# Performance work log

Measured on AMD Instinct MI355X. Metric: run time of the kernel, lower is better.

## Reference

```python
import jax, jax.numpy as jnp
import numpy as np

NUM_HEADS = 8
EPS = 1e-6


def hamilton(a, b):
    # Quaternion (Hamilton) product on the last axis (size 4), broadcasting leading dims.
    aw, ax, ay, az = a[..., 0], a[..., 1], a[..., 2], a[..., 3]
    bw, bx, by, bz = b[..., 0], b[..., 1], b[..., 2], b[..., 3]
    return jnp.stack([
        aw * bw - ax * bx - ay * by - az * bz,
        aw * bx + ax * bw + ay * bz - az * by,
        aw * by - ax * bz + ay * bw + az * bx,
        aw * bz + ax * by - ay * bx + az * bw,
    ], axis=-1)


def setup_inputs() -> dict:
    key = jax.random.key(0)
    ks = jax.random.split(key, 7)
    B, L, E = 2, 384, 512
    s = 1.0 / np.sqrt(E)
    return {
        'x': jax.random.normal(ks[0], (B, L, E), dtype=jnp.float32),
        'Wq': jax.random.normal(ks[1], (E, E), dtype=jnp.float32) * s,
        'Wk': jax.random.normal(ks[2], (E, E), dtype=jnp.float32) * s,
        'Wv': jax.random.normal(ks[3], (E, E), dtype=jnp.float32) * s,
        'Wo': jax.random.normal(ks[4], (E, E), dtype=jnp.float32) * s,
        'dde_w': jax.random.normal(ks[5], (4, 4), dtype=jnp.float32) * 0.5,
        'dde_b': jnp.zeros((4,), dtype=jnp.float32),
    }


def reference(x, Wq, Wk, Wv, Wo, dde_w, dde_b):
    B, L, E = x.shape
    H = NUM_HEADS
    hd = E // H            # head_dim
    c = hd // 4            # quaternion atoms per head

    def proj_quat(W):
        # x @ W^T  -> split heads -> quaternion atoms: (B*H, L, c, 4)
        y = jnp.einsum('ble,fe->blf', x, W)
        y = y.reshape(B, L, H, hd).transpose(0, 2, 1, 3)  # (B,H,L,hd)
        return y.reshape(B * H, L, c, 4)

    q = proj_quat(Wq)
    k = proj_quat(Wk)
    v = proj_quat(Wv)

    # Broadcasted Hamilton product: (BH, L, L, c, 4)
    interference = hamilton(q[:, :, None, :, :], k[:, None, :, :, :])
    norm = jnp.linalg.norm(interference, axis=-1, keepdims=True) + EPS
    spinor = interference / norm

    # Discrete decision gate: mean over atoms -> (BH, L, L, 4) -> sigmoid(linear)
    gate_in = spinor.mean(axis=-2)
    gate = jax.nn.sigmoid(jnp.einsum('blmq,pq->blmp', gate_in, dde_w) + dde_b)
    spinor = spinor * gate[:, :, :, None, :]

    # Value aggregation: Hamilton product with v, summed over key positions j
    ctx = hamilton(spinor, v[:, None, :, :, :]).sum(axis=2)  # (BH, L, c, 4)

    ctx = ctx.reshape(B, H, L, hd).transpose(0, 2, 1, 3).reshape(B, L, E)
    return jnp.einsum('ble,fe->blf', ctx, Wo)
```

## Files before the change

kernel.cpp:

```cpp
#include <hip/hip_runtime.h>
#include <math.h>

#define L_SEQ 384
#define E_DIM 512
#define NHEAD 8
#define NBH   16
#define HD    64
#define LOG2E 1.44269504f

typedef __attribute__((ext_vector_type(8))) __bf16 bf16x8;
typedef __attribute__((ext_vector_type(8))) _Float16 f16x8;
typedef __attribute__((ext_vector_type(4))) float f32x4;

union u4h8 { uint4 u; f16x8 h; };

__device__ __forceinline__ float uniform_f(float v) {
  return __uint_as_float(__builtin_amdgcn_readfirstlane(__float_as_uint(v)));
}

__device__ __forceinline__ unsigned f2bf(float f) {
  unsigned u = __float_as_uint(f);
  return (u + 0x7FFFu + ((u >> 16) & 1u)) >> 16;
}

__device__ __forceinline__ unsigned ror16(unsigned x) { return (x >> 16) | (x << 16); }

__device__ __forceinline__ float dpp_xor1(float x) {
  return __int_as_float(__builtin_amdgcn_mov_dpp(__float_as_int(x), 0xB1, 0xF, 0xF, 0));
}
__device__ __forceinline__ float dpp_xor2(float x) {
  return __int_as_float(__builtin_amdgcn_mov_dpp(__float_as_int(x), 0x4E, 0xF, 0xF, 0));
}
template <int IMM>
__device__ __forceinline__ float swz_xor(float x) {
  return __int_as_float(__builtin_amdgcn_ds_swizzle(__float_as_int(x), IMM));
}

__device__ __forceinline__ size_t pidx(int row, int k, int Kd) {
  return ((((size_t)(row >> 4) * (Kd >> 5) + (k >> 5)) * 4 + ((k >> 3) & 3)) * 16
          + (row & 15)) * 8 + (k & 7);
}

__global__ __launch_bounds__(256) void to_bf16_all(
    const float* __restrict__ x, const float* __restrict__ Wq,
    const float* __restrict__ Wk, const float* __restrict__ Wv,
    const float* __restrict__ Wo, unsigned short* __restrict__ dst1,
    unsigned short* __restrict__ dst2, float* __restrict__ outz)
{
  int e0 = (blockIdx.x * 256 + threadIdx.x) * 4;
  if (e0 >= 1835008) return;
  if (e0 >= 1441792) {
    *(float4*)(outz + (e0 - 1441792)) = make_float4(0.f, 0.f, 0.f, 0.f);
    return;
  }
  const float* src; unsigned short* d; int s;
  if (e0 < 393216)       { src = x;  s = e0;           d = dst1; }
  else if (e0 < 655360)  { src = Wq; s = e0 - 393216;  d = dst1 + 393216; }
  else if (e0 < 917504)  { src = Wk; s = e0 - 655360;  d = dst1 + 655360; }
  else if (e0 < 1179648) { src = Wv; s = e0 - 917504;  d = dst1 + 917504; }
  else                   { src = Wo; s = e0 - 1179648; d = dst2; }
  float4 v = *(const float4*)(src + s);
  unsigned lo = f2bf(v.x) | (f2bf(v.y) << 16);
  unsigned hi = f2bf(v.z) | (f2bf(v.w) << 16);
  int row = s >> 9, k = s & 511;
  *(uint2*)(d + pidx(row, k, 512)) = make_uint2(lo, hi);
}

template <int NTN, int MODE>
__global__ __launch_bounds__(256) void gemm_mfma(
    const __bf16* __restrict__ A, const __bf16* __restrict__ B0,
    const __bf16* __restrict__ B1, const __bf16* __restrict__ B2,
    float* __restrict__ C0, float* __restrict__ C1, float* __restrict__ C2,
    int M, int N, int K)
{
  const int z = blockIdx.z;
  const __bf16* Bm = (MODE == 2) ? B0 : (z == 0) ? B0 : (z == 1) ? B1 : B2;
  float* Cp = (MODE == 2) ? C0 : (z == 0) ? C0 : (z == 1) ? C1 : C2;

  const int tid = threadIdx.x;
  const int wave = tid >> 6, lane = tid & 63;
  const int m0 = blockIdx.y * 64 + wave * 16;
  const int n0 = blockIdx.x * (16 * NTN);
  const int mr = lane & 15, quad = lane >> 4;
  const int KT = K >> 5;
  const int kb0 = (MODE == 2) ? z * 4 : 0;
  const int KL = (MODE == 2) ? 4 : KT;

  f32x4 acc[NTN];
  #pragma unroll
  for (int nt = 0; nt < NTN; ++nt) acc[nt] = (f32x4){0.f, 0.f, 0.f, 0.f};

  const __bf16* ap = A + ((size_t)(m0 >> 4) * KT + kb0) * 512 + lane * 8;
  const __bf16* bp = Bm + ((size_t)(n0 >> 4) * KT + kb0) * 512 + lane * 8;

  #pragma unroll 4
  for (int ks = 0; ks < KL; ++ks) {
    bf16x8 a = *(const bf16x8*)(ap + (size_t)ks * 512);
    #pragma unroll
    for (int nt = 0; nt < NTN; ++nt) {
      bf16x8 b = *(const bf16x8*)(bp + ((size_t)nt * KT + ks) * 512);
      acc[nt] = __builtin_amdgcn_mfma_f32_16x16x32_bf16(a, b, acc[nt], 0, 0, 0);
    }
  }

  if (MODE == 2) {
    #pragma unroll
    for (int nt = 0; nt < NTN; ++nt) {
      int n = n0 + nt * 16 + mr;
      #pragma unroll
      for (int r = 0; r < 4; ++r) {
        int m = m0 + quad * 4 + r;
        __hip_atomic_fetch_add(&Cp[(size_t)m * N + n], acc[nt][r],
                               __ATOMIC_RELAXED, __HIP_MEMORY_SCOPE_AGENT);
      }
    }
  } else {
    _Float16* Hp = (_Float16*)Cp;
    #pragma unroll
    for (int nt = 0; nt < NTN; ++nt) {
      int n = n0 + nt * 16 + mr;
      #pragma unroll
      for (int r = 0; r < 4; ++r) {
        float val = acc[nt][r];
        float s = val * val;
        s += dpp_xor1(s);
        s += dpp_xor2(s);
        float sc = (z == 2) ? 1.f : __builtin_amdgcn_rsqf(fmaxf(s, 1e-30f));
        int m = m0 + quad * 4 + r;
        int b = m / L_SEQ, l = m - b * L_SEQ;
        int row = (b * NHEAD + (n >> 6)) * L_SEQ + l;
        Hp[pidx(row, n & 63, 64)] = (_Float16)(val * sc);
      }
    }
  }
}

__global__ __launch_bounds__(256) void z_build(
    const _Float16* __restrict__ khh, const _Float16* __restrict__ vhh,
    _Float16* __restrict__ Z0)
{
  const int tid = threadIdx.x;
  const int l = blockIdx.x * 64 + (tid & 63);
  const int a = blockIdx.y * 4 + (tid >> 6);
  const int bh = blockIdx.z;

  size_t off = pidx(bh * L_SEQ + l, a * 4, 64);
  union { uint2 u; _Float16 h[4]; } kk, vv;
  kk.u = *(const uint2*)(khh + off);
  vv.u = *(const uint2*)(vhh + off);

  float kb[4] = {(float)kk.h[0], (float)kk.h[1], (float)kk.h[2], (float)kk.h[3]};
  float ve[4] = {(float)vv.h[0], (float)vv.h[1], (float)vv.h[2], (float)vv.h[3]};
  _Float16* zp = Z0 + (size_t)bh * (256 * 384);
  #pragma unroll
  for (int b = 0; b < 4; ++b)
    #pragma unroll
    for (int e = 0; e < 4; ++e)
      zp[pidx(a * 16 + b * 4 + e, l, 384)] = (_Float16)(kb[b] * ve[e]);
}

__global__ __launch_bounds__(256) void score_gate(
    const _Float16* __restrict__ qhh, const _Float16* __restrict__ khh,
    const float* __restrict__ dde_w, const float* __restrict__ dde_b,
    _Float16* __restrict__ G)
{
  const int tid = threadIdx.x, wave = tid >> 6, lane = tid & 63;
  const int mr = lane & 15, quad = lane >> 4;
  const int bh = blockIdx.z;
  const int i0 = blockIdx.y * 64 + wave * 16;
  const int j0 = blockIdx.x * 32;

  float wn[16], bn[4];
  #pragma unroll
  for (int t = 0; t < 16; ++t) wn[t] = uniform_f(dde_w[t]) * (-LOG2E * 0.0625f);
  #pragma unroll
  for (int c = 0; c < 4; ++c) bn[c] = uniform_f(dde_b[c]) * (-LOG2E);

  f32x4 acc[4][2];
  #pragma unroll
  for (int c = 0; c < 4; ++c)
    #pragma unroll
    for (int nt = 0; nt < 2; ++nt) acc[c][nt] = (f32x4){0.f, 0.f, 0.f, 0.f};

  const _Float16* ap = qhh + (size_t)((bh * L_SEQ + i0) >> 4) * 2 * 512 + lane * 8;
  const _Float16* bp = khh + (size_t)((bh * L_SEQ + j0) >> 4) * 2 * 512 + lane * 8;

  #pragma unroll
  for (int ks = 0; ks < 2; ++ks) {
    uint4 qa = *(const uint4*)(ap + ks * 512);
    unsigned s0 = ror16(qa.x), s1 = ror16(qa.y), s2 = ror16(qa.z), s3 = ror16(qa.w);
    u4h8 fr[4];
    fr[0].u = make_uint4(qa.x ^ 0x80000000u, qa.y ^ 0x80008000u,
                         qa.z ^ 0x80000000u, qa.w ^ 0x80008000u);
    fr[1].u = make_uint4(s0, s1 ^ 0x00008000u, s2, s3 ^ 0x00008000u);
    fr[2].u = make_uint4(qa.y, qa.x ^ 0x80000000u, qa.w, qa.z ^ 0x80000000u);
    fr[3].u = make_uint4(s1 ^ 0x80000000u, s0, s3 ^ 0x80000000u, s2);
    #pragma unroll
    for (int nt = 0; nt < 2; ++nt) {
      u4h8 bb; bb.h = *(const f16x8*)(bp + ((size_t)nt * 2 + ks) * 512);
      #pragma unroll
      for (int c = 0; c < 4; ++c)
        acc[c][nt] = __builtin_amdgcn_mfma_f32_16x16x32_f16(fr[c].h, bb.h, acc[c][nt], 0, 0, 0);
    }
  }

  #pragma unroll
  for (int nt = 0; nt < 2; ++nt) {
    const int j = j0 + nt * 16 + mr;
    #pragma unroll
    for (int r = 0; r < 4; ++r) {
      const int i = i0 + quad * 4 + r;
      float S0 = acc[0][nt][r], S1 = acc[1][nt][r];
      float S2 = acc[2][nt][r], S3 = acc[3][nt][r];
      #pragma unroll
      for (int c = 0; c < 4; ++c) {
        float n = bn[c] + wn[c*4+0]*S0 + wn[c*4+1]*S1 + wn[c*4+2]*S2 + wn[c*4+3]*S3;
        float g = __builtin_amdgcn_rcpf(1.f + __builtin_amdgcn_exp2f(n));
        G[(size_t)(c * NBH + bh) * (384 * 384) + pidx(i, j, 384)] = (_Float16)g;
      }
    }
  }
}

__global__ __launch_bounds__(256) void pv_combine(
    const _Float16* __restrict__ G, const _Float16* __restrict__ Z0,
    const _Float16* __restrict__ qhh, unsigned short* __restrict__ CTXB)
{
  __shared__ float qs[16][17];
  __shared__ float vxs[4][4][16][4];
  const int tid = threadIdx.x, c = tid >> 6, lane = tid & 63;
  const int mr = lane & 15, quad = lane >> 4;
  const int bh = blockIdx.z;
  const int i0 = blockIdx.x * 16;
  const int cg = blockIdx.y;

  {
    int il = tid >> 4, t = tid & 15;
    qs[il][t] = (float)qhh[pidx(bh * L_SEQ + i0 + il, cg * 16 + t, 64)];
  }
  __syncthreads();

  const int bq = mr >> 2, e = mr & 3;
  const unsigned msk =
      ((((0x284Eu >> (c * 4 + bq)) ^ (0xC6A0u >> (c * 4 + e))) & 1u) << 31);

  f32x4 acc[4];
  #pragma unroll
  for (int nt = 0; nt < 4; ++nt) acc[nt] = (f32x4){0.f, 0.f, 0.f, 0.f};

  const _Float16* apg = G + (size_t)(c * NBH + bh) * (384 * 384)
                          + (size_t)(i0 >> 4) * 12 * 512 + lane * 8;
  const _Float16* bpz = Z0 + (size_t)bh * (256 * 384)
                           + (size_t)(cg * 4) * 12 * 512 + lane * 8;

  #pragma unroll 4
  for (int ks = 0; ks < 12; ++ks) {
    u4h8 aa; aa.h = *(const f16x8*)(apg + (size_t)ks * 512);
    #pragma unroll
    for (int nt = 0; nt < 4; ++nt) {
      u4h8 bb; bb.h = *(const f16x8*)(bpz + ((size_t)nt * 12 + ks) * 512);
      acc[nt] = __builtin_amdgcn_mfma_f32_16x16x32_f16(aa.h, bb.h, acc[nt], 0, 0, 0);
    }
  }

  #pragma unroll
  for (int nt = 0; nt < 4; ++nt) {
    #pragma unroll
    for (int r = 0; r < 4; ++r) {
      int il = quad * 4 + r;
      float sq = __uint_as_float(__float_as_uint(qs[il][nt * 4 + (bq ^ c)]) ^ msk);
      float v = sq * acc[nt][r];
      v += swz_xor<0x101F>(v);
      v += swz_xor<0x201F>(v);
      if (bq == 0) vxs[c][e][il][nt] = v;
    }
  }
  __syncthreads();

  {
    int il = tid >> 4, cc = tid & 15, nt = cc >> 2, d = cc & 3;
    float s = vxs[0][d][il][nt] + vxs[1][1 ^ d][il][nt] +
              vxs[2][2 ^ d][il][nt] + vxs[3][3 ^ d][il][nt];
    int bb_ = bh >> 3, hh = bh & 7;
    CTXB[pidx(bb_ * L_SEQ + i0 + il, hh * HD + cg * 16 + nt * 4 + d, 512)] =
        (unsigned short)f2bf(s);
  }
}

extern "C" void kernel_launch(void* const* d_in, const int* in_sizes, int n_in,
                              void* d_out, int out_size, void* d_ws, size_t ws_size,
                              hipStream_t stream)
{
  const float* x     = (const float*)d_in[0];
  const float* Wq    = (const float*)d_in[1];
  const float* Wk    = (const float*)d_in[2];
  const float* Wv    = (const float*)d_in[3];
  const float* Wo    = (const float*)d_in[4];
  const float* dde_w = (const float*)d_in[5];
  const float* dde_b = (const float*)d_in[6];
  float* out = (float*)d_out;

  char* ws = (char*)d_ws;
  unsigned short* Wob  = (unsigned short*)(ws + 0);
  _Float16* qhh = (_Float16*)(ws + 524288);
  _Float16* khh = (_Float16*)(ws + 1310720);
  unsigned short* CTXB = (unsigned short*)(ws + 1310720);
  _Float16* Z0h = (_Float16*)(ws + 2097152);
  _Float16* Gh  = (_Float16*)(ws + 5242880);
  _Float16* vhh = (_Float16*)(ws + 5242880);
  unsigned short* xb  = (unsigned short*)(ws + 6029312);
  unsigned short* Wqb = (unsigned short*)(ws + 6815744);
  unsigned short* Wkb = (unsigned short*)(ws + 7340032);
  unsigned short* Wvb = (unsigned short*)(ws + 7864320);

  to_bf16_all<<<1792, 256, 0, stream>>>(x, Wq, Wk, Wv, Wo, xb, Wob, out);

  gemm_mfma<2, 1><<<dim3(16, 12, 3), 256, 0, stream>>>(
      (const __bf16*)xb, (const __bf16*)Wqb, (const __bf16*)Wkb, (const __bf16*)Wvb,
      (float*)qhh, (float*)khh, (float*)vhh, 2 * L_SEQ, E_DIM, E_DIM);

  z_build<<<dim3(6, 4, 16), 256, 0, stream>>>(khh, vhh, Z0h);

  score_gate<<<dim3(12, 6, 16), 256, 0, stream>>>(qhh, khh, dde_w, dde_b, Gh);

  pv_combine<<<dim3(24, 4, 16), 256, 0, stream>>>(Gh, Z0h, qhh, CTXB);

  gemm_mfma<2, 2><<<dim3(16, 12, 4), 256, 0, stream>>>(
      (const __bf16*)CTXB, (const __bf16*)Wob, nullptr, nullptr,
      out, nullptr, nullptr, 2 * L_SEQ, E_DIM, E_DIM);
}
```

Before: 112.2 us.

## Fuse score-gate and PV combine into one kernel with gates in LDS

Merges the score_gate and pv_combine kernels so each block computes the sigmoid gate tile for its 16 query rows chunk by chunk into shared memory and feeds it straight into the PV MFMAs. This removes the global gate tensor of shape 4x16x384x384 in fp16 and its write/read round trip, plus one launch. In exchange the score MFMAs are recomputed once per column group (4x redundant) and two barriers are added per chunk. The QKV projection GEMM tile config is also changed to launch twice as many blocks.

```diff
diff --git a/kernel.cpp b/kernel.cpp
--- a/kernel.cpp
+++ b/kernel.cpp
@@ -159,16 +159,24 @@
       zp[pidx(a * 16 + b * 4 + e, l, 384)] = (_Float16)(kb[b] * ve[e]);
 }
 
-__global__ __launch_bounds__(256) void score_gate(
+__global__ __launch_bounds__(256) void gate_pv(
     const _Float16* __restrict__ qhh, const _Float16* __restrict__ khh,
-    const float* __restrict__ dde_w, const float* __restrict__ dde_b,
-    _Float16* __restrict__ G)
-{
-  const int tid = threadIdx.x, wave = tid >> 6, lane = tid & 63;
+    const _Float16* __restrict__ Z0, const float* __restrict__ dde_w,
+    const float* __restrict__ dde_b, unsigned short* __restrict__ CTXB)
+{
+  __shared__ _Float16 gbuf[4096];
+  __shared__ float vxs[4][4][16][4];
+  __shared__ float qs[16][17];
+
+  const int tid = threadIdx.x, w = tid >> 6, lane = tid & 63;
   const int mr = lane & 15, quad = lane >> 4;
-  const int bh = blockIdx.z;
-  const int i0 = blockIdx.y * 64 + wave * 16;
-  const int j0 = blockIdx.x * 32;
+  const int bh = blockIdx.z, cg = blockIdx.y, ib = blockIdx.x;
+  const int i0 = ib * 16;
+
+  {
+    int il = tid >> 4, t = tid & 15;
+    qs[il][t] = (float)qhh[pidx(bh * L_SEQ + i0 + il, cg * 16 + t, 64)];
+  }
 
   float wn[16], bn[4];
   #pragma unroll
@@ -176,91 +184,73 @@
   #pragma unroll
   for (int c = 0; c < 4; ++c) bn[c] = uniform_f(dde_b[c]) * (-LOG2E);
 
-  f32x4 acc[4][2];
-  #pragma unroll
-  for (int c = 0; c < 4; ++c)
-    #pragma unroll
-    for (int nt = 0; nt < 2; ++nt) acc[c][nt] = (f32x4){0.f, 0.f, 0.f, 0.f};
-
-  const _Float16* ap = qhh + (size_t)((bh * L_SEQ + i0) >> 4) * 2 * 512 + lane * 8;
-  const _Float16* bp = khh + (size_t)((bh * L_SEQ + j0) >> 4) * 2 * 512 + lane * 8;
-
-  #pragma unroll
-  for (int ks = 0; ks < 2; ++ks) {
-    uint4 qa = *(const uint4*)(ap + ks * 512);
-    unsigned s0 = ror16(qa.x), s1 = ror16(qa.y), s2 = ror16(qa.z), s3 = ror16(qa.w);
-    u4h8 fr[4];
-    fr[0].u = make_uint4(qa.x ^ 0x80000000u, qa.y ^ 0x80008000u,
-                         qa.z ^ 0x80000000u, qa.w ^ 0x80008000u);
-    fr[1].u = make_uint4(s0, s1 ^ 0x00008000u, s2, s3 ^ 0x00008000u);
-    fr[2].u = make_uint4(qa.y, qa.x ^ 0x80000000u, qa.w, qa.z ^ 0x80000000u);
-    fr[3].u = make_uint4(s1 ^ 0x80000000u, s0, s3 ^ 0x80000000u, s2);
-    #pragma unroll
-    for (int nt = 0; nt < 2; ++nt) {
-      u4h8 bb; bb.h = *(const f16x8*)(bp + ((size_t)nt * 2 + ks) * 512);
-      #pragma unroll
-      for (int c = 0; c < 4; ++c)
-        acc[c][nt] = __builtin_amdgcn_mfma_f32_16x16x32_f16(fr[c].h, bb.h, acc[c][nt], 0, 0, 0);
-    }
-  }
-
-  #pragma unroll
-  for (int nt = 0; nt < 2; ++nt) {
-    const int j = j0 + nt * 16 + mr;
+  u4h8 fr[4][2];
+  {
+    const _Float16* ap = qhh + ((size_t)(bh * 24 + ib)) * 2 * 512 + lane * 8;
+    #pragma unroll
+    for (int ks = 0; ks < 2; ++ks) {
+      uint4 qa = *(const uint4*)(ap + ks * 512);
+      unsigned s0 = ror16(qa.x), s1 = ror16(qa.y), s2 = ror16(qa.z), s3 = ror16(qa.w);
+      fr[0][ks].u = make_uint4(qa.x ^ 0x80000000u, qa.y ^ 0x80008000u,
+                               qa.z ^ 0x80000000u, qa.w ^ 0x80008000u);
+      fr[1][ks].u = make_uint4(s0, s1 ^ 0x00008000u, s2, s3 ^ 0x00008000u);
+      fr[2][ks].u = make_uint4(qa.y, qa.x ^ 0x80000000u, qa.w, qa.z ^ 0x80000000u);
+      fr[3][ks].u = make_uint4(s1 ^ 0x80000000u, s0, s3 ^ 0x80000000u, s2);
+    }
+  }
+
+  const int bq = mr >> 2, e = mr & 3;
+  const unsigned msk =
+      ((((0x284Eu >> (w * 4 + bq)) ^ (0xC6A0u >> (w * 4 + e))) & 1u) << 31);
+
+  f32x4 acc[4];
+  #pragma unroll
+  for (int nt = 0; nt < 4; ++nt) acc[nt] = (f32x4){0.f, 0.f, 0.f, 0.f};
+
+  const int jl = w * 16 + mr;
+  const int gw = (jl >> 3) * 128 + (jl & 7) + quad * 32;
+
+  for (int ch = 0; ch < 6; ++ch) {
+    u4h8 zb[2][4];
+    #pragma unroll
+    for (int ks2 = 0; ks2 < 2; ++ks2)
+      #pragma unroll
+      for (int nt = 0; nt < 4; ++nt)
+        zb[ks2][nt].h = *(const f16x8*)(Z0 + (size_t)bh * (256 * 384)
+                         + (((size_t)(cg * 4 + nt) * 12 + ch * 2 + ks2) * 512) + lane * 8);
+
+    const _Float16* bp = khh + ((size_t)(bh * 24 + ch * 4 + w)) * 2 * 512 + lane * 8;
+    u4h8 kb[2];
+    kb[0].h = *(const f16x8*)(bp);
+    kb[1].h = *(const f16x8*)(bp + 512);
+    f32x4 accS[4];
+    #pragma unroll
+    for (int c = 0; c < 4; ++c) {
+      accS[c] = (f32x4){0.f, 0.f, 0.f, 0.f};
+      accS[c] = __builtin_amdgcn_mfma_f32_16x16x32_f16(fr[c][0].h, kb[0].h, accS[c], 0, 0, 0);
+      accS[c] = __builtin_amdgcn_mfma_f32_16x16x32_f16(fr[c][1].h, kb[1].h, accS[c], 0, 0, 0);
+    }
+
     #pragma unroll
     for (int r = 0; r < 4; ++r) {
-      const int i = i0 + quad * 4 + r;
-      float S0 = acc[0][nt][r], S1 = acc[1][nt][r];
-      float S2 = acc[2][nt][r], S3 = acc[3][nt][r];
+      float S0 = accS[0][r], S1 = accS[1][r], S2 = accS[2][r], S3 = accS[3][r];
       #pragma unroll
       for (int c = 0; c < 4; ++c) {
         float n = bn[c] + wn[c*4+0]*S0 + wn[c*4+1]*S1 + wn[c*4+2]*S2 + wn[c*4+3]*S3;
         float g = __builtin_amdgcn_rcpf(1.f + __builtin_amdgcn_exp2f(n));
-        G[(size_t)(c * NBH + bh) * (384 * 384) + pidx(i, j, 384)] = (_Float16)g;
+        gbuf[c * 1024 + gw + r * 8] = (_Float16)g;
       }
     }
-  }
-}
-
-__global__ __launch_bounds__(256) void pv_combine(
-    const _Float16* __restrict__ G, const _Float16* __restrict__ Z0,
-    const _Float16* __restrict__ qhh, unsigned short* __restrict__ CTXB)
-{
-  __shared__ float qs[16][17];
-  __shared__ float vxs[4][4][16][4];
-  const int tid = threadIdx.x, c = tid >> 6, lane = tid & 63;
-  const int mr = lane & 15, quad = lane >> 4;
-  const int bh = blockIdx.z;
-  const int i0 = blockIdx.x * 16;
-  const int cg = blockIdx.y;
-
-  {
-    int il = tid >> 4, t = tid & 15;
-    qs[il][t] = (float)qhh[pidx(bh * L_SEQ + i0 + il, cg * 16 + t, 64)];
-  }
-  __syncthreads();
-
-  const int bq = mr >> 2, e = mr & 3;
-  const unsigned msk =
-      ((((0x284Eu >> (c * 4 + bq)) ^ (0xC6A0u >> (c * 4 + e))) & 1u) << 31);
-
-  f32x4 acc[4];
-  #pragma unroll
-  for (int nt = 0; nt < 4; ++nt) acc[nt] = (f32x4){0.f, 0.f, 0.f, 0.f};
-
-  const _Float16* apg = G + (size_t)(c * NBH + bh) * (384 * 384)
-                          + (size_t)(i0 >> 4) * 12 * 512 + lane * 8;
-  const _Float16* bpz = Z0 + (size_t)bh * (256 * 384)
-                           + (size_t)(cg * 4) * 12 * 512 + lane * 8;
-
-  #pragma unroll 4
-  for (int ks = 0; ks < 12; ++ks) {
-    u4h8 aa; aa.h = *(const f16x8*)(apg + (size_t)ks * 512);
-    #pragma unroll
-    for (int nt = 0; nt < 4; ++nt) {
-      u4h8 bb; bb.h = *(const f16x8*)(bpz + ((size_t)nt * 12 + ks) * 512);
-      acc[nt] = __builtin_amdgcn_mfma_f32_16x16x32_f16(aa.h, bb.h, acc[nt], 0, 0, 0);
-    }
+    __syncthreads();
+
+    #pragma unroll
+    for (int ks2 = 0; ks2 < 2; ++ks2) {
+      f16x8 aa = *(const f16x8*)&gbuf[(w * 2 + ks2) * 512 + lane * 8];
+      #pragma unroll
+      for (int nt = 0; nt < 4; ++nt)
+        acc[nt] = __builtin_amdgcn_mfma_f32_16x16x32_f16(aa, zb[ks2][nt].h, acc[nt], 0, 0, 0);
+    }
+    __syncthreads();
   }
 
   #pragma unroll
@@ -268,11 +258,11 @@
     #pragma unroll
     for (int r = 0; r < 4; ++r) {
       int il = quad * 4 + r;
-      float sq = __uint_as_float(__float_as_uint(qs[il][nt * 4 + (bq ^ c)]) ^ msk);
+      float sq = __uint_as_float(__float_as_uint(qs[il][nt * 4 + (bq ^ w)]) ^ msk);
       float v = sq * acc[nt][r];
       v += swz_xor<0x101F>(v);
       v += swz_xor<0x201F>(v);
-      if (bq == 0) vxs[c][e][il][nt] = v;
+      if (bq == 0) vxs[w][e][il][nt] = v;
     }
   }
   __syncthreads();
@@ -304,10 +294,9 @@
   unsigned short* Wob  = (unsigned short*)(ws + 0);
   _Float16* qhh = (_Float16*)(ws + 524288);
   _Float16* khh = (_Float16*)(ws + 1310720);
-  unsigned short* CTXB = (unsigned short*)(ws + 1310720);
   _Float16* Z0h = (_Float16*)(ws + 2097152);
-  _Float16* Gh  = (_Float16*)(ws + 5242880);
   _Float16* vhh = (_Float16*)(ws + 5242880);
+  unsigned short* CTXB = (unsigned short*)(ws + 5242880);
   unsigned short* xb  = (unsigned short*)(ws + 6029312);
   unsigned short* Wqb = (unsigned short*)(ws + 6815744);
   unsigned short* Wkb = (unsigned short*)(ws + 7340032);
@@ -315,15 +304,13 @@
 
   to_bf16_all<<<1792, 256, 0, stream>>>(x, Wq, Wk, Wv, Wo, xb, Wob, out);
 
-  gemm_mfma<2, 1><<<dim3(16, 12, 3), 256, 0, stream>>>(
+  gemm_mfma<1, 1><<<dim3(32, 12, 3), 256, 0, stream>>>(
       (const __bf16*)xb, (const __bf16*)Wqb, (const __bf16*)Wkb, (const __bf16*)Wvb,
       (float*)qhh, (float*)khh, (float*)vhh, 2 * L_SEQ, E_DIM, E_DIM);
 
   z_build<<<dim3(6, 4, 16), 256, 0, stream>>>(khh, vhh, Z0h);
 
-  score_gate<<<dim3(12, 6, 16), 256, 0, stream>>>(qhh, khh, dde_w, dde_b, Gh);
-
-  pv_combine<<<dim3(24, 4, 16), 256, 0, stream>>>(Gh, Z0h, qhh, CTXB);
+  gate_pv<<<dim3(24, 4, 16), 256, 0, stream>>>(qhh, khh, Z0h, dde_w, dde_b, CTXB);
 
   gemm_mfma<2, 2><<<dim3(16, 12, 4), 256, 0, stream>>>(
       (const __bf16*)CTXB, (const __bf16*)Wob, nullptr, nullptr,
```

Result: no change. 110.1 us (-1.9%).
